# Kernel tuning notes

Measured on AMD Instinct MI355X. Metric: run time of the kernel, lower is better.

The kernel has to match this reference:

```python
import jax, jax.numpy as jnp
import numpy as np

BETA = 0.25

def _encoder(x, W0, b0, W1, b1, W2, b2):
    # MLP: Linear+ReLU, Linear+ReLU, Linear (dims 768->512->256->64)
    h = jax.nn.relu(x @ W0 + b0)
    h = jax.nn.relu(h @ W1 + b1)
    return h @ W2 + b2

def _rvq(z, codebooks):
    # Residual vector quantization over L=4 levels (structurally distinct loop).
    residual = z
    x_q = jnp.zeros_like(z)
    losses = []
    codes = []
    for l in range(codebooks.shape[0]):
        cb = codebooks[l]  # [K, e]
        # squared L2 distances [N, K] via expansion (avoids materializing [N,K,e])
        d = (jnp.sum(residual * residual, axis=1, keepdims=True)
             - 2.0 * residual @ cb.T
             + jnp.sum(cb * cb, axis=1))
        idx = jnp.argmin(d, axis=1)           # [N]
        q = cb[idx]                            # gather [N, e]
        # codebook loss + beta * commitment loss
        loss = (jnp.mean((jax.lax.stop_gradient(q) - residual) ** 2)
                + BETA * jnp.mean((q - jax.lax.stop_gradient(residual)) ** 2))
        losses.append(loss)
        # straight-through estimator
        q_st = residual + jax.lax.stop_gradient(q - residual)
        residual = residual - q_st
        x_q = x_q + q_st
        codes.append(idx)
    rq_loss = jnp.mean(jnp.stack(losses))
    return x_q, rq_loss, jnp.stack(codes)  # codes: [L, N] int


def setup_inputs() -> dict:
    key = jax.random.key(0)
    ks = jax.random.split(key, 8)
    N, D = 131072, 768
    dims = [768, 512, 256, 64]
    x = jax.random.normal(ks[0], (N, D), dtype=jnp.float32)
    W0 = jax.random.normal(ks[1], (dims[0], dims[1]), dtype=jnp.float32) * (1.0 / np.sqrt(dims[0]))
    b0 = jnp.zeros((dims[1],), dtype=jnp.float32)
    W1 = jax.random.normal(ks[2], (dims[1], dims[2]), dtype=jnp.float32) * (1.0 / np.sqrt(dims[1]))
    b1 = jnp.zeros((dims[2],), dtype=jnp.float32)
    W2 = jax.random.normal(ks[3], (dims[2], dims[3]), dtype=jnp.float32) * (1.0 / np.sqrt(dims[2]))
    b2 = jnp.zeros((dims[3],), dtype=jnp.float32)
    codebooks = jax.random.normal(ks[4], (4, 256, 64), dtype=jnp.float32)
    return {"x": x, "W0": W0, "b0": b0, "W1": W1, "b1": b1, "W2": W2, "b2": b2,
            "codebooks": codebooks}


def reference(x, W0, b0, W1, b1, W2, b2, codebooks):
    z = _encoder(x, W0, b0, W1, b1, W2, b2)          # [N, 64]
    x_q, rq_loss, codes = _rvq(z, codebooks)
    return x_q, rq_loss, codes
```

## Files before the change

### kernel.cpp

```cpp
#include <hip/hip_runtime.h>
#include <hip/hip_bf16.h>


typedef double d2v __attribute__((ext_vector_type(2)));

template<bool RELU>
__global__ __launch_bounds__(256) void gemm128(
    const float* __restrict__ A, const float* __restrict__ W,
    const float* __restrict__ bias, float* __restrict__ C,
    int M, int N, int K)
{
    __shared__ float As[16][132];
    __shared__ float Bs[16][132];

    const int tid = threadIdx.x;
    const int tx = tid & 15;
    const int ty = tid >> 4;
    const int col0 = blockIdx.x * 128;
    const int row0 = blockIdx.y * 128;

    const float* Ab = A + (size_t)row0 * K;
    const float* Wb = W + col0;

    const int am0 = tid >> 2,          ak0 = (tid & 3) * 4;
    const int am1 = (tid + 256) >> 2,  ak1 = ((tid + 256) & 3) * 4;
    const int bk0 = tid >> 5,          bn0 = (tid & 31) * 4;
    const int bk1 = (tid + 256) >> 5,  bn1 = ((tid + 256) & 31) * 4;

    float acc[8][8] = {};

    float4 sa0 = *reinterpret_cast<const float4*>(Ab + (size_t)am0 * K + ak0);
    float4 sa1 = *reinterpret_cast<const float4*>(Ab + (size_t)am1 * K + ak1);
    float4 sb0 = *reinterpret_cast<const float4*>(Wb + (size_t)bk0 * N + bn0);
    float4 sb1 = *reinterpret_cast<const float4*>(Wb + (size_t)bk1 * N + bn1);
    As[ak0 + 0][am0] = sa0.x; As[ak0 + 1][am0] = sa0.y;
    As[ak0 + 2][am0] = sa0.z; As[ak0 + 3][am0] = sa0.w;
    As[ak1 + 0][am1] = sa1.x; As[ak1 + 1][am1] = sa1.y;
    As[ak1 + 2][am1] = sa1.z; As[ak1 + 3][am1] = sa1.w;
    *reinterpret_cast<float4*>(&Bs[bk0][bn0]) = sb0;
    *reinterpret_cast<float4*>(&Bs[bk1][bn1]) = sb1;
    __syncthreads();

    for (int k0 = 0; k0 < K; k0 += 16) {
        const bool hasNext = (k0 + 16 < K);
        if (hasNext) {
            const float* An = Ab + k0 + 16;
            const float* Wn = Wb + (size_t)(k0 + 16) * N;
            sa0 = *reinterpret_cast<const float4*>(An + (size_t)am0 * K + ak0);
            sa1 = *reinterpret_cast<const float4*>(An + (size_t)am1 * K + ak1);
            sb0 = *reinterpret_cast<const float4*>(Wn + (size_t)bk0 * N + bn0);
            sb1 = *reinterpret_cast<const float4*>(Wn + (size_t)bk1 * N + bn1);
        }

#pragma unroll
        for (int kk = 0; kk < 16; ++kk) {
            float4 a0 = *reinterpret_cast<const float4*>(&As[kk][ty * 4]);
            float4 a1 = *reinterpret_cast<const float4*>(&As[kk][64 + ty * 4]);
            float4 b0 = *reinterpret_cast<const float4*>(&Bs[kk][tx * 4]);
            float4 b1 = *reinterpret_cast<const float4*>(&Bs[kk][64 + tx * 4]);
            float ar[8] = {a0.x, a0.y, a0.z, a0.w, a1.x, a1.y, a1.z, a1.w};
            float br[8] = {b0.x, b0.y, b0.z, b0.w, b1.x, b1.y, b1.z, b1.w};
#pragma unroll
            for (int m = 0; m < 8; ++m)
#pragma unroll
                for (int n = 0; n < 8; ++n)
                    acc[m][n] = fmaf(ar[m], br[n], acc[m][n]);
        }

        if (hasNext) {
            __syncthreads();
            As[ak0 + 0][am0] = sa0.x; As[ak0 + 1][am0] = sa0.y;
            As[ak0 + 2][am0] = sa0.z; As[ak0 + 3][am0] = sa0.w;
            As[ak1 + 0][am1] = sa1.x; As[ak1 + 1][am1] = sa1.y;
            As[ak1 + 2][am1] = sa1.z; As[ak1 + 3][am1] = sa1.w;
            *reinterpret_cast<float4*>(&Bs[bk0][bn0]) = sb0;
            *reinterpret_cast<float4*>(&Bs[bk1][bn1]) = sb1;
            __syncthreads();
        }
    }

    float bl[4], bh[4];
#pragma unroll
    for (int n = 0; n < 4; ++n) {
        bl[n] = bias[col0 + tx * 4 + n];
        bh[n] = bias[col0 + 64 + tx * 4 + n];
    }
#pragma unroll
    for (int half = 0; half < 2; ++half) {
#pragma unroll
        for (int r = 0; r < 4; ++r) {
            int m = half * 4 + r;
            int row = row0 + half * 64 + ty * 4 + r;
            float4 lo, hi;
            lo.x = acc[m][0] + bl[0]; lo.y = acc[m][1] + bl[1];
            lo.z = acc[m][2] + bl[2]; lo.w = acc[m][3] + bl[3];
            hi.x = acc[m][4] + bh[0]; hi.y = acc[m][5] + bh[1];
            hi.z = acc[m][6] + bh[2]; hi.w = acc[m][7] + bh[3];
            if (RELU) {
                lo.x = fmaxf(lo.x, 0.f); lo.y = fmaxf(lo.y, 0.f);
                lo.z = fmaxf(lo.z, 0.f); lo.w = fmaxf(lo.w, 0.f);
                hi.x = fmaxf(hi.x, 0.f); hi.y = fmaxf(hi.y, 0.f);
                hi.z = fmaxf(hi.z, 0.f); hi.w = fmaxf(hi.w, 0.f);
            }
            float* Cr = C + (size_t)row * N + col0;
            *reinterpret_cast<float4*>(Cr + tx * 4) = lo;
            *reinterpret_cast<float4*>(Cr + 64 + tx * 4) = hi;
        }
    }
}

template<bool RELU>
__global__ __launch_bounds__(256) void gemm_bias(
    const float* __restrict__ A, const float* __restrict__ W,
    const float* __restrict__ bias, float* __restrict__ C,
    int M, int N, int K)
{
    __shared__ float As[16][132];
    __shared__ float Bs[16][68];

    const int tid = threadIdx.x;
    const int tx = tid & 15;
    const int ty = tid >> 4;
    const int col0 = blockIdx.x * 64;
    const int row0 = blockIdx.y * 128;

    const float* Ab = A + (size_t)row0 * K;
    const float* Wb = W + col0;

    float acc[8][4] = {};

    for (int k0 = 0; k0 < K; k0 += 16) {
#pragma unroll
        for (int i = 0; i < 2; ++i) {
            int pos = tid + i * 256;
            int m  = pos >> 2;
            int k4 = (pos & 3) * 4;
            float4 v = *reinterpret_cast<const float4*>(Ab + (size_t)m * K + k0 + k4);
            As[k4 + 0][m] = v.x; As[k4 + 1][m] = v.y;
            As[k4 + 2][m] = v.z; As[k4 + 3][m] = v.w;
        }
        {
            int kk = tid >> 4;
            int n4 = (tid & 15) * 4;
            float4 v = *reinterpret_cast<const float4*>(Wb + (size_t)(k0 + kk) * N + n4);
            *reinterpret_cast<float4*>(&Bs[kk][n4]) = v;
        }
        __syncthreads();
#pragma unroll
        for (int kk = 0; kk < 16; ++kk) {
            float4 a0 = *reinterpret_cast<const float4*>(&As[kk][ty * 8]);
            float4 a1 = *reinterpret_cast<const float4*>(&As[kk][ty * 8 + 4]);
            float4 bv = *reinterpret_cast<const float4*>(&Bs[kk][tx * 4]);
            float a[8] = {a0.x, a0.y, a0.z, a0.w, a1.x, a1.y, a1.z, a1.w};
            float b[4] = {bv.x, bv.y, bv.z, bv.w};
#pragma unroll
            for (int m = 0; m < 8; ++m)
#pragma unroll
                for (int n = 0; n < 4; ++n)
                    acc[m][n] = fmaf(a[m], b[n], acc[m][n]);
        }
        __syncthreads();
    }

    float bv[4];
#pragma unroll
    for (int n = 0; n < 4; ++n) bv[n] = bias[col0 + tx * 4 + n];
#pragma unroll
    for (int m = 0; m < 8; ++m) {
        int row = row0 + ty * 8 + m;
        float4 o;
        float v0 = acc[m][0] + bv[0];
        float v1 = acc[m][1] + bv[1];
        float v2 = acc[m][2] + bv[2];
        float v3 = acc[m][3] + bv[3];
        if (RELU) {
            v0 = fmaxf(v0, 0.f); v1 = fmaxf(v1, 0.f);
            v2 = fmaxf(v2, 0.f); v3 = fmaxf(v3, 0.f);
        }
        o.x = v0; o.y = v1; o.z = v2; o.w = v3;
        *reinterpret_cast<float4*>(C + (size_t)row * N + col0 + tx * 4) = o;
    }
}

__global__ void cb_norms(const float* __restrict__ cb,
                         double* __restrict__ cn64, float* __restrict__ cnf) {
    int c = blockIdx.x * 64 + threadIdx.x;
    const float* p = cb + (size_t)c * 64;
    double s = 0.0;
#pragma unroll
    for (int j = 0; j < 64; ++j) {
        double v = (double)p[j];
        s = fma(v, v, s);
    }
    cn64[c] = s;
    cnf[c]  = (float)s;
}

__global__ void build_cbw(const float* __restrict__ cb, double* __restrict__ cbw) {
    int i = blockIdx.x * 256 + threadIdx.x;
    cbw[i] = -2.0 * (double)cb[i];
}

#define EGUARD 1e-3

__device__ __forceinline__ double rank64(const double* __restrict__ p,
                                         double R0, const float (&rd)[64]) {
    double c0 = 0.0, c1 = 0.0, c2 = 0.0, c3 = 0.0;
#pragma unroll
    for (int j = 0; j < 16; ++j) {
        d2v x = *reinterpret_cast<const d2v*>(p + j * 4);
        d2v y = *reinterpret_cast<const d2v*>(p + j * 4 + 2);
        c0 = fma(x[0], (double)rd[j * 4 + 0], c0);
        c1 = fma(x[1], (double)rd[j * 4 + 1], c1);
        c2 = fma(y[0], (double)rd[j * 4 + 2], c2);
        c3 = fma(y[1], (double)rd[j * 4 + 3], c3);
    }
    return R0 + ((c0 + c1) + (c2 + c3));
}

__global__ __launch_bounds__(256, 2) void rvq_v5(
    const float* __restrict__ z,
    const float* __restrict__ cbf,
    const double* __restrict__ cbw,
    const double* __restrict__ cn64,
    const float* __restrict__ cnf,
    float* __restrict__ xq,
    float* __restrict__ codes,
    double* __restrict__ partials,
    int row0, int Ntot)
{
    __shared__ float sd1[4][64];
    __shared__ float sd2[4][64];
    __shared__ int   si1[4][64];
    __shared__ int   si2[4][64];

    const int tid  = threadIdx.x;
    const int lane = tid & 63;
    const int w    = tid >> 6;
    const int wu   = __builtin_amdgcn_readfirstlane(w);
    const int blk  = blockIdx.x;
    const int grow0 = row0 + blk * 64;

    float rd[64];
    const float* zr = z + (size_t)(blk * 64 + lane) * 64;
#pragma unroll
    for (int q = 0; q < 16; ++q) {
        float4 v = *reinterpret_cast<const float4*>(zr + q * 4);
        rd[q * 4 + 0] = v.x; rd[q * 4 + 1] = v.y;
        rd[q * 4 + 2] = v.z; rd[q * 4 + 3] = v.w;
    }

    double sse = 0.0;

    for (int lv = 0; lv < 4; ++lv) {
        const int cbase = lv * 256;
        __syncthreads();

        const float* cwl = cbf + (size_t)(cbase + wu * 64) * 64;
        const float* cnl = cnf + cbase + wu * 64;

        float d1 = 3.4e38f, d2 = 3.4e38f;
        int   i1 = 0,       i2 = 0;

#pragma unroll 1
        for (int c = 0; c < 64; ++c) {
            const float* cp = cwl + c * 64;
            float acc8[8];
#pragma unroll
            for (int q = 0; q < 8; ++q) {
                float4 va = *reinterpret_cast<const float4*>(cp + q * 8);
                float4 vb = *reinterpret_cast<const float4*>(cp + q * 8 + 4);
                float t = 0.f;
                t = fmaf(va.x, rd[q * 8 + 0], t);
                t = fmaf(va.y, rd[q * 8 + 1], t);
                t = fmaf(va.z, rd[q * 8 + 2], t);
                t = fmaf(va.w, rd[q * 8 + 3], t);
                t = fmaf(vb.x, rd[q * 8 + 4], t);
                t = fmaf(vb.y, rd[q * 8 + 5], t);
                t = fmaf(vb.z, rd[q * 8 + 6], t);
                t = fmaf(vb.w, rd[q * 8 + 7], t);
                acc8[q] = t;
            }
            float dot = ((acc8[0] + acc8[1]) + (acc8[2] + acc8[3]))
                      + ((acc8[4] + acc8[5]) + (acc8[6] + acc8[7]));
            float d = fmaf(-2.f, dot, cnl[c]);
            int code = wu * 64 + c;
            if (d < d1) { d2 = d1; i2 = i1; d1 = d; i1 = code; }
            else if (d < d2) { d2 = d; i2 = code; }
        }

        sd1[w][lane] = d1; si1[w][lane] = i1;
        sd2[w][lane] = d2; si2[w][lane] = i2;
        __syncthreads();

        float bd1 = sd1[0][lane]; int bi1 = si1[0][lane]; int wstar = 0;
#pragma unroll
        for (int ww = 1; ww < 4; ++ww) {
            float dd = sd1[ww][lane]; int ii = si1[ww][lane];
            if (dd < bd1 || (dd == bd1 && ii < bi1)) { bd1 = dd; bi1 = ii; wstar = ww; }
        }
        float d2g = 3.4e38f; int i2g = 0;
#pragma unroll
        for (int ww = 0; ww < 4; ++ww) {
            float dd = (ww == wstar) ? sd2[ww][lane] : sd1[ww][lane];
            int   ii = (ww == wstar) ? si2[ww][lane] : si1[ww][lane];
            if (dd < d2g) { d2g = dd; i2g = ii; }
        }

        double R1 = rank64(cbw + (size_t)(cbase + bi1) * 64, cn64[cbase + bi1], rd);
        double R2 = rank64(cbw + (size_t)(cbase + i2g) * 64, cn64[cbase + i2g], rd);
        int ci; double Rw;
        if (R1 < R2 || (R1 == R2 && bi1 < i2g)) { ci = bi1; Rw = R1; }
        else                                    { ci = i2g; Rw = R2; }

        if (!(Rw < (double)d2g - EGUARD)) {
            float l8f = fminf(fminf(sd2[0][lane], sd2[1][lane]),
                              fminf(sd2[2][lane], sd2[3][lane]));
            double L8 = (double)l8f;
            double Rm = 1.0e300; int im = 0;
#pragma unroll
            for (int ww = 0; ww < 4; ++ww) {
#pragma unroll
                for (int k = 0; k < 2; ++k) {
                    int cc = k ? si2[ww][lane] : si1[ww][lane];
                    double R = rank64(cbw + (size_t)(cbase + cc) * 64,
                                      cn64[cbase + cc], rd);
                    if (R < Rm || (R == Rm && cc < im)) { Rm = R; im = cc; }
                }
            }
            if (Rm < L8 - EGUARD) {
                ci = im;
            } else {
                double dmin = 1.0e300; int imin = 0;
#pragma unroll 1
                for (int c = 0; c < 256; ++c) {
                    double R = rank64(cbw + (size_t)(cbase + c) * 64,
                                      cn64[cbase + c], rd);
                    if (R < dmin) { dmin = R; imin = c; }
                }
                ci = imin;
            }
        }

        const float* qp = cbf + (size_t)(cbase + ci) * 64;
        double lsse = 0.0;
#pragma unroll
        for (int q = 0; q < 16; ++q) {
            float4 qv = *reinterpret_cast<const float4*>(qp + q * 4);
            float r0 = rd[q * 4 + 0], r1 = rd[q * 4 + 1];
            float r2 = rd[q * 4 + 2], r3 = rd[q * 4 + 3];
            if (w == 0) {
                float e0 = qv.x - r0, e1 = qv.y - r1;
                float e2 = qv.z - r2, e3 = qv.w - r3;
                lsse = fma((double)e0, (double)e0, lsse);
                lsse = fma((double)e1, (double)e1, lsse);
                lsse = fma((double)e2, (double)e2, lsse);
                lsse = fma((double)e3, (double)e3, lsse);
            }
            rd[q * 4 + 0] = r0 - qv.x; rd[q * 4 + 1] = r1 - qv.y;
            rd[q * 4 + 2] = r2 - qv.z; rd[q * 4 + 3] = r3 - qv.w;
        }
        if (w == 0) {
            sse += lsse;
            codes[(size_t)lv * Ntot + grow0 + lane] = (float)ci;
        }
    }

    if (w == 0) {
        size_t base = (size_t)(grow0 + lane) * 64;
#pragma unroll
        for (int q = 0; q < 16; ++q) {
            float4 zv = *reinterpret_cast<const float4*>(zr + q * 4);
            float4 o;
            o.x = zv.x - rd[q * 4 + 0];
            o.y = zv.y - rd[q * 4 + 1];
            o.z = zv.z - rd[q * 4 + 2];
            o.w = zv.w - rd[q * 4 + 3];
            *reinterpret_cast<float4*>(xq + base + q * 4) = o;
        }
        double s = sse;
#pragma unroll
        for (int off = 32; off > 0; off >>= 1) {
            union { double d; int i[2]; } u; u.d = s;
            u.i[0] = __shfl_down(u.i[0], off, 64);
            u.i[1] = __shfl_down(u.i[1], off, 64);
            s += u.d;
        }
        if (lane == 0) partials[grow0 >> 6] = s;
    }
}

__global__ void loss_final(const double* __restrict__ partials, int n,
                           float* __restrict__ out, double scale) {
    __shared__ double s[256];
    double acc = 0.0;
    for (int i = threadIdx.x; i < n; i += 256) acc += partials[i];
    s[threadIdx.x] = acc;
    __syncthreads();
    for (int off = 128; off > 0; off >>= 1) {
        if ((int)threadIdx.x < off) s[threadIdx.x] += s[threadIdx.x + off];
        __syncthreads();
    }
    if (threadIdx.x == 0) *out = (float)(s[0] * scale);
}

extern "C" void kernel_launch(void* const* d_in, const int* in_sizes, int n_in,
                              void* d_out, int out_size, void* d_ws, size_t ws_size,
                              hipStream_t stream) {
    const float* x  = (const float*)d_in[0];
    const float* W0 = (const float*)d_in[1];
    const float* b0 = (const float*)d_in[2];
    const float* W1 = (const float*)d_in[3];
    const float* b1 = (const float*)d_in[4];
    const float* W2 = (const float*)d_in[5];
    const float* b2 = (const float*)d_in[6];
    const float* cb = (const float*)d_in[7];

    const int N = in_sizes[0] / 768;

    float* out   = (float*)d_out;
    float* xq    = out;
    float* loss  = out + (size_t)N * 64;
    float* codes = loss + 1;

    const int nblk_total = N / 64;
    const size_t tail_floats = 131072 + 2048 + 2 * (size_t)nblk_total + 1024 + 64;

    size_t avail = ws_size / 4;
    avail = (avail > tail_floats) ? (avail - tail_floats) : 0;
    int Nc = (int)(avail / 832);
    Nc = (Nc / 128) * 128;
    if (Nc > N) Nc = N;
    if (Nc < 128) Nc = 128;

    float* ws = (float*)d_ws;
    float* h0 = ws;
    float* h1 = h0 + (size_t)Nc * 512;
    float* z  = h1 + (size_t)Nc * 256;
    double* cbw      = (double*)(ws + (size_t)Nc * 832);
    double* cn64     = cbw + 65536;
    double* partials = cn64 + 1024;
    float*  cnf      = (float*)(partials + nblk_total);

    cb_norms <<<16, 64, 0, stream>>>(cb, cn64, cnf);
    build_cbw<<<256, 256, 0, stream>>>(cb, cbw);

    for (int r0 = 0; r0 < N; r0 += Nc) {
        int cur = (N - r0 < Nc) ? (N - r0) : Nc;
        gemm128<true ><<<dim3(512 / 128, cur / 128), 256, 0, stream>>>(
            x + (size_t)r0 * 768, W0, b0, h0, cur, 512, 768);
        gemm128<true ><<<dim3(256 / 128, cur / 128), 256, 0, stream>>>(
            h0, W1, b1, h1, cur, 256, 512);
        gemm_bias<false><<<dim3(1, cur / 128), 256, 0, stream>>>(
            h1, W2, b2, z, cur, 64, 256);
        rvq_v5<<<cur / 64, 256, 0, stream>>>(
            z, cb, cbw, cn64, cnf, xq, codes, partials, r0, N);
    }

    loss_final<<<1, 256, 0, stream>>>(partials, nblk_total, loss,
                                      1.25 / (4.0 * (double)N * 64.0));
}
```

Before: 2.668 ms.

## Remap GEMM workgroups per XCD and stage RVQ codebook chunks in LDS

The FP32 GEMMs now use a 1D grid and remap block IDs so consecutive tiles land on the same XCD chiplet, improving L2 reuse of A rows across column tiles. The RVQ kernel now stages codebook chunks of 32 codes per wave into shared memory in two chunks per level, instead of reading them from global memory per lane. Its launch bound rises to 4 blocks per CU to allow higher occupancy. In exchange the RVQ kernel adds extra barriers and 32KB of LDS per block, which may limit occupancy, and the higher launch bound pushes the compiler toward fewer registers, which could cause spills given the 64-float residual held in registers.

```diff
diff --git a/kernel.cpp b/kernel.cpp
--- a/kernel.cpp
+++ b/kernel.cpp
@@ -4,7 +4,7 @@
 
 typedef double d2v __attribute__((ext_vector_type(2)));
 
-template<bool RELU>
+template<bool RELU, int NCOLSHIFT>
 __global__ __launch_bounds__(256) void gemm128(
     const float* __restrict__ A, const float* __restrict__ W,
     const float* __restrict__ bias, float* __restrict__ C,
@@ -13,11 +13,20 @@
     __shared__ float As[16][132];
     __shared__ float Bs[16][132];
 
+    const int nwg  = gridDim.x;
+    const int b    = blockIdx.x;
+    const int xcd  = b & 7;
+    const int rest = b >> 3;
+    const int q8   = nwg >> 3, r8 = nwg & 7;
+    const int wg   = (xcd < r8 ? xcd * (q8 + 1) : r8 * (q8 + 1) + (xcd - r8) * q8) + rest;
+    const int NCOL = 1 << NCOLSHIFT;
+
+    const int col0 = (wg & (NCOL - 1)) * 128;
+    const int row0 = (wg >> NCOLSHIFT) * 128;
+
     const int tid = threadIdx.x;
     const int tx = tid & 15;
     const int ty = tid >> 4;
-    const int col0 = blockIdx.x * 128;
-    const int row0 = blockIdx.y * 128;
 
     const float* Ab = A + (size_t)row0 * K;
     const float* Wb = W + col0;
@@ -218,7 +227,7 @@
     return R0 + ((c0 + c1) + (c2 + c3));
 }
 
-__global__ __launch_bounds__(256, 2) void rvq_v5(
+__global__ __launch_bounds__(256, 4) void rvq_v6(
     const float* __restrict__ z,
     const float* __restrict__ cbf,
     const double* __restrict__ cbw,
@@ -229,6 +238,7 @@
     double* __restrict__ partials,
     int row0, int Ntot)
 {
+    __shared__ float cbs[4][32][64];
     __shared__ float sd1[4][64];
     __shared__ float sd2[4][64];
     __shared__ int   si1[4][64];
@@ -254,39 +264,53 @@
 
     for (int lv = 0; lv < 4; ++lv) {
         const int cbase = lv * 256;
-        __syncthreads();
-
-        const float* cwl = cbf + (size_t)(cbase + wu * 64) * 64;
-        const float* cnl = cnf + cbase + wu * 64;
 
         float d1 = 3.4e38f, d2 = 3.4e38f;
         int   i1 = 0,       i2 = 0;
 
+#pragma unroll
+        for (int ch = 0; ch < 2; ++ch) {
+#pragma unroll
+            for (int i = 0; i < 8; ++i) {
+                int f  = tid + i * 256;
+                int sw = f >> 9;
+                int cc = (f >> 4) & 31;
+                int qq = f & 15;
+                float4 v = *reinterpret_cast<const float4*>(
+                    cbf + ((size_t)(cbase + sw * 64 + ch * 32 + cc)) * 64 + qq * 4);
+                *reinterpret_cast<float4*>(&cbs[sw][cc][qq * 4]) = v;
+            }
+            __syncthreads();
+
+            const float* cw  = &cbs[wu][0][0];
+            const float* cnl = cnf + cbase + wu * 64 + ch * 32;
 #pragma unroll 1
-        for (int c = 0; c < 64; ++c) {
-            const float* cp = cwl + c * 64;
-            float acc8[8];
-#pragma unroll
-            for (int q = 0; q < 8; ++q) {
-                float4 va = *reinterpret_cast<const float4*>(cp + q * 8);
-                float4 vb = *reinterpret_cast<const float4*>(cp + q * 8 + 4);
-                float t = 0.f;
-                t = fmaf(va.x, rd[q * 8 + 0], t);
-                t = fmaf(va.y, rd[q * 8 + 1], t);
-                t = fmaf(va.z, rd[q * 8 + 2], t);
-                t = fmaf(va.w, rd[q * 8 + 3], t);
-                t = fmaf(vb.x, rd[q * 8 + 4], t);
-                t = fmaf(vb.y, rd[q * 8 + 5], t);
-                t = fmaf(vb.z, rd[q * 8 + 6], t);
-                t = fmaf(vb.w, rd[q * 8 + 7], t);
-                acc8[q] = t;
-            }
-            float dot = ((acc8[0] + acc8[1]) + (acc8[2] + acc8[3]))
-                      + ((acc8[4] + acc8[5]) + (acc8[6] + acc8[7]));
-            float d = fmaf(-2.f, dot, cnl[c]);
-            int code = wu * 64 + c;
-            if (d < d1) { d2 = d1; i2 = i1; d1 = d; i1 = code; }
-            else if (d < d2) { d2 = d; i2 = code; }
+            for (int c = 0; c < 32; ++c) {
+                const float* cp = cw + c * 64;
+                float acc8[8];
+#pragma unroll
+                for (int q = 0; q < 8; ++q) {
+                    float4 va = *reinterpret_cast<const float4*>(cp + q * 8);
+                    float4 vb = *reinterpret_cast<const float4*>(cp + q * 8 + 4);
+                    float t = 0.f;
+                    t = fmaf(va.x, rd[q * 8 + 0], t);
+                    t = fmaf(va.y, rd[q * 8 + 1], t);
+                    t = fmaf(va.z, rd[q * 8 + 2], t);
+                    t = fmaf(va.w, rd[q * 8 + 3], t);
+                    t = fmaf(vb.x, rd[q * 8 + 4], t);
+                    t = fmaf(vb.y, rd[q * 8 + 5], t);
+                    t = fmaf(vb.z, rd[q * 8 + 6], t);
+                    t = fmaf(vb.w, rd[q * 8 + 7], t);
+                    acc8[q] = t;
+                }
+                float dot = ((acc8[0] + acc8[1]) + (acc8[2] + acc8[3]))
+                          + ((acc8[4] + acc8[5]) + (acc8[6] + acc8[7]));
+                float d = fmaf(-2.f, dot, cnl[c]);
+                int code = wu * 64 + ch * 32 + c;
+                if (d < d1) { d2 = d1; i2 = i1; d1 = d; i1 = code; }
+                else if (d < d2) { d2 = d; i2 = code; }
+            }
+            __syncthreads();
         }
 
         sd1[w][lane] = d1; si1[w][lane] = i1;
@@ -364,6 +388,7 @@
             sse += lsse;
             codes[(size_t)lv * Ntot + grow0 + lane] = (float)ci;
         }
+        __syncthreads();
     }
 
     if (w == 0) {
@@ -447,13 +472,13 @@
 
     for (int r0 = 0; r0 < N; r0 += Nc) {
         int cur = (N - r0 < Nc) ? (N - r0) : Nc;
-        gemm128<true ><<<dim3(512 / 128, cur / 128), 256, 0, stream>>>(
+        gemm128<true, 2><<<4 * (cur / 128), 256, 0, stream>>>(
             x + (size_t)r0 * 768, W0, b0, h0, cur, 512, 768);
-        gemm128<true ><<<dim3(256 / 128, cur / 128), 256, 0, stream>>>(
+        gemm128<true, 1><<<2 * (cur / 128), 256, 0, stream>>>(
             h0, W1, b1, h1, cur, 256, 512);
         gemm_bias<false><<<dim3(1, cur / 128), 256, 0, stream>>>(
             h1, W2, b2, z, cur, 64, 256);
-        rvq_v5<<<cur / 64, 256, 0, stream>>>(
+        rvq_v6<<<cur / 64, 256, 0, stream>>>(
             z, cb, cbw, cn64, cnf, xq, codes, partials, r0, N);
     }
 
```

Result: slower. 3.002 ms (+12.5%).
